# Optimization experiments

Measured on AMD Instinct MI355X. Metric: run time of the kernel, lower is better.

The kernel has to match this reference:

```python
import jax, jax.numpy as jnp
import numpy as np

TEMPERATURE = 10000.0
LN_EPS = 1e-5

def build_freqs(H, W, head_dim):
    # (H*W, head_dim) rotary angles: [theta_h, theta_h, theta_w, theta_w]
    gh, gw = jnp.meshgrid(jnp.arange(H, dtype=jnp.float32), jnp.arange(W, dtype=jnp.float32), indexing='ij')
    dq = head_dim // 4
    freq = 1.0 / (TEMPERATURE ** (jnp.arange(dq, dtype=jnp.float32) / dq))
    th = gh.reshape(-1, 1) * freq[None, :]
    tw = gw.reshape(-1, 1) * freq[None, :]
    return jnp.concatenate([th, th, tw, tw], axis=-1)

def apply_rope(x, freqs):
    # x: (B, nh, N, hd), freqs: (N, hd)
    cos = jnp.cos(freqs)[None, None]
    sin = jnp.sin(freqs)[None, None]
    hd = x.shape[-1]
    x1, x2 = x[..., :hd // 2], x[..., hd // 2:]
    x_rot = jnp.concatenate([-x2, x1], axis=-1)
    return x * cos + x_rot * sin

def setup_inputs() -> dict:
    key = jax.random.key(0)
    ks = jax.random.split(key, 8)
    dim, hidden, B, H, W = 192, 384, 4, 128, 128
    N = H * W
    s = 0.02
    return {
        'x': jax.random.normal(ks[0], (B, N, dim), jnp.float32),
        'in_w': jax.random.normal(ks[1], (hidden, dim), jnp.float32) * s,
        'in_b': jnp.zeros((hidden,), jnp.float32),
        'qkv_w': jax.random.normal(ks[2], (3 * hidden, hidden), jnp.float32) * s,
        'qkv_b': jnp.zeros((3 * hidden,), jnp.float32),
        'lepe_w': jax.random.normal(ks[3], (hidden, 1, 3, 3), jnp.float32) * s,
        'lepe_b': jnp.zeros((hidden,), jnp.float32),
        'ln_g': jnp.ones((hidden,), jnp.float32),
        'ln_b': jnp.zeros((hidden,), jnp.float32),
        'out_w': jax.random.normal(ks[4], (dim, hidden), jnp.float32) * s,
        'out_b': jnp.zeros((dim,), jnp.float32),
        'H': H,
        'W': W,
    }

def reference(x, in_w, in_b, qkv_w, qkv_b, lepe_w, lepe_b, ln_g, ln_b, out_w, out_b, H, W):
    B, N, C = x.shape
    hidden = in_w.shape[0]
    nh = 8
    hd = hidden // nh
    # in_proj: 1x1 conv == per-token linear
    x_seq = jnp.einsum('bnc,hc->bnh', x, in_w) + in_b
    # fused qkv
    qkv = jnp.einsum('bnh,oh->bno', x_seq, qkv_w) + qkv_b
    q, k, v = jnp.split(qkv, 3, axis=-1)
    # LEPE: 3x3 depthwise conv on V in NCHW layout
    v2d = v.transpose(0, 2, 1).reshape(B, hidden, H, W)
    lepe = jax.lax.conv_general_dilated(
        v2d, lepe_w, window_strides=(1, 1), padding=((1, 1), (1, 1)),
        feature_group_count=hidden, dimension_numbers=('NCHW', 'OIHW', 'NCHW'))
    lepe = lepe + lepe_b[None, :, None, None]
    v = v + lepe.reshape(B, hidden, N).transpose(0, 2, 1)
    # split heads -> (B, nh, N, hd)
    q = q.reshape(B, N, nh, hd).transpose(0, 2, 1, 3)
    k = k.reshape(B, N, nh, hd).transpose(0, 2, 1, 3)
    v = v.reshape(B, N, nh, hd).transpose(0, 2, 1, 3)
    freqs = build_freqs(H, W, hd)
    q = apply_rope(q, freqs)
    k = apply_rope(k, freqs)
    # phi = ELU + 1 feature map
    q = jax.nn.elu(q) + 1.0
    k = jax.nn.elu(k) + 1.0
    # linear attention associativity trick
    kv = jnp.einsum('bhnd,bhne->bhde', k, v)
    out = jnp.einsum('bhnd,bhde->bhne', q, kv)
    k_sum = k.sum(axis=2)  # (B, nh, hd)
    denom = jnp.maximum(jnp.einsum('bhnd,bhd->bhn', q, k_sum)[..., None], 1e-6)
    out = out / denom
    out = out.transpose(0, 2, 1, 3).reshape(B, N, hidden)
    # LayerNorm + out_proj
    mu = out.mean(axis=-1, keepdims=True)
    var = out.var(axis=-1, keepdims=True)
    out = (out - mu) * jax.lax.rsqrt(var + LN_EPS) * ln_g + ln_b
    return jnp.einsum('bnh,ch->bnc', out, out_w) + out_b
```

## Files before the change

kernel.cpp:

```cpp
#include <hip/hip_runtime.h>
#include <cstdint>
#include <cstddef>

#define NN_TOK 16384
#define ROWS   65536
#define CDIM   192
#define HID    384
#define NHEAD  8
#define HD     48
#define QKVO   1152

typedef unsigned short ushort_t;
typedef __bf16 bf16x8 __attribute__((ext_vector_type(8)));
typedef float  f32x4  __attribute__((ext_vector_type(4)));

__device__ __forceinline__ ushort_t f2bf(float f) {
  __bf16 h = (__bf16)f;
  ushort_t u;
  __builtin_memcpy(&u, &h, 2);
  return u;
}
__device__ __forceinline__ float bf2f(ushort_t u) {
  return __uint_as_float(((unsigned int)u) << 16);
}

__global__ void cast_x(const float* __restrict__ x, ushort_t* __restrict__ xb, int n8) {
  int i = blockIdx.x * blockDim.x + threadIdx.x;
  if (i >= n8) return;
  const float4* src = (const float4*)(x + (size_t)i * 8);
  float4 f0 = src[0], f1 = src[1];
  uint4 pk;
  pk.x = (unsigned)f2bf(f0.x) | ((unsigned)f2bf(f0.y) << 16);
  pk.y = (unsigned)f2bf(f0.z) | ((unsigned)f2bf(f0.w) << 16);
  pk.z = (unsigned)f2bf(f1.x) | ((unsigned)f2bf(f1.y) << 16);
  pk.w = (unsigned)f2bf(f1.z) | ((unsigned)f2bf(f1.w) << 16);
  *(uint4*)(xb + (size_t)i * 8) = pk;
}

__global__ void combine_w(const float* __restrict__ in_w, const float* __restrict__ in_b,
                          const float* __restrict__ qkv_w, const float* __restrict__ qkv_b,
                          ushort_t* __restrict__ Wcb, float* __restrict__ bc) {
  int o = blockIdx.x;
  int c = threadIdx.x;
  const float* qw = qkv_w + o * HID;
  float s = 0.f;
  for (int m = 0; m < HID; ++m) s += qw[m] * in_w[m * CDIM + c];
  Wcb[o * CDIM + c] = f2bf(s);
  if (c == 0) {
    float sb = qkv_b[o];
    for (int m = 0; m < HID; ++m) sb += qw[m] * in_b[m];
    bc[o] = sb;
  }
}

__global__ void cast_owT(const float* __restrict__ w, ushort_t* __restrict__ wt, int n) {
  int i = blockIdx.x * blockDim.x + threadIdx.x;
  if (i >= n) return;
  int j = i & 7, rest = i >> 3;
  int l15 = rest & 15; rest >>= 4;
  int quad = rest & 3; rest >>= 2;
  int kt = rest % 12, ct = rest / 12;
  int col = ct * 16 + l15, k = kt * 32 + quad * 8 + j;
  wt[i] = f2bf(w[col * HID + k]);
}

__global__ void build_tab(float4* __restrict__ tab4) {
  int i = blockIdx.x * blockDim.x + threadIdx.x;
  if (i >= NN_TOK * 24) return;
  int n = i / 24, dp = i - n * 24;
  int j = dp % 12;
  const float c0 = 1.1073093649624542f;
  float freq = exp2f(-(float)j * c0);
  float fy = (float)(n >> 7), fx = (float)(n & 127);
  float s1, c1, s2, c2;
  sincosf(fy * freq, &s1, &c1);
  sincosf(fx * freq, &s2, &c2);
  tab4[i] = make_float4(c1, s1, c2, s2);
}

template<int BM, int BN, int WM, int WN, bool OUTBF16>
__global__ __launch_bounds__(256) void gemm_mfma(const ushort_t* __restrict__ A, int lda,
                                                 const ushort_t* __restrict__ Wb,
                                                 const float* __restrict__ bias,
                                                 void* __restrict__ Cptr,
                                                 int K, int O, int nbx) {
  constexpr int TM = BM / WM / 16;
  constexpr int TN = BN / WN / 16;
  __shared__ __align__(16) ushort_t As[BM][40];
  __shared__ __align__(16) ushort_t Bs[BN][40];
  const int t    = threadIdx.x;
  const int lane = t & 63;
  const int wave = t >> 6;
  const int quad = lane >> 4;
  const int l15  = lane & 15;
  const int wm   = wave / WN, wn = wave % WN;
  const int m_base = wm * (BM / WM);
  const int n_base = wn * (BN / WN);
  const int cpx = gridDim.x >> 3;
  const int id  = blockIdx.x;
  const int swz = (id & 7) * cpx + (id >> 3);
  const int o0  = (swz % nbx) * BN;
  const int n0  = (swz / nbx) * BM;
  f32x4 acc[TM][TN] = {};

  for (int kt = 0; kt < K; kt += 32) {
    for (int c = t; c < BM * 4; c += 256) {
      int row = c >> 2, col8 = (c & 3) * 8;
      *(uint4*)&As[row][col8] = *(const uint4*)(A + (size_t)(n0 + row) * lda + kt + col8);
    }
    for (int c = t; c < BN * 4; c += 256) {
      int row = c >> 2, col8 = (c & 3) * 8;
      *(uint4*)&Bs[row][col8] = *(const uint4*)(Wb + (size_t)(o0 + row) * K + kt + col8);
    }
    __syncthreads();
    bf16x8 af[TM], bfr[TN];
#pragma unroll
    for (int mi = 0; mi < TM; ++mi)
      af[mi] = *(const bf16x8*)&As[m_base + mi * 16 + l15][quad * 8];
#pragma unroll
    for (int ni = 0; ni < TN; ++ni)
      bfr[ni] = *(const bf16x8*)&Bs[n_base + ni * 16 + l15][quad * 8];
#pragma unroll
    for (int mi = 0; mi < TM; ++mi)
#pragma unroll
      for (int ni = 0; ni < TN; ++ni)
        acc[mi][ni] = __builtin_amdgcn_mfma_f32_16x16x32_bf16(af[mi], bfr[ni], acc[mi][ni], 0, 0, 0);
    __syncthreads();
  }
#pragma unroll
  for (int mi = 0; mi < TM; ++mi) {
#pragma unroll
    for (int ni = 0; ni < TN; ++ni) {
      int col = o0 + n_base + ni * 16 + l15;
      float bv = bias[col];
      int rbase = n0 + m_base + mi * 16 + quad * 4;
#pragma unroll
      for (int r = 0; r < 4; ++r) {
        float val = acc[mi][ni][r] + bv;
        if (OUTBF16) ((ushort_t*)Cptr)[(size_t)(rbase + r) * O + col] = f2bf(val);
        else         ((float*)Cptr)[(size_t)(rbase + r) * O + col] = val;
      }
    }
  }
}

__device__ __forceinline__ int fragEl(int pg, int nb, int dd, int nm) {
  return pg * 2200 + nb * 136 + dd * 8 + nm;
}

__global__ __launch_bounds__(256) void kv_partial_k(const ushort_t* __restrict__ kq,
                                                    const ushort_t* __restrict__ vq,
                                                    const float4* __restrict__ tab4,
                                                    const float* __restrict__ lw,
                                                    const float* __restrict__ lb,
                                                    float* __restrict__ part) {
  const int bid   = blockIdx.x;
  const int chunk = bid & 63;
  const int bh    = bid >> 6;
  const int b     = bh >> 3;
  const int h     = bh & 7;
  const int t     = threadIdx.x;
  const int lane  = t & 63;
  const int wave  = t >> 6;
  __shared__ __align__(16) ushort_t ksR[3 * 2200];
  __shared__ __align__(16) ushort_t vsR[4 * 2200];
  __shared__ __align__(16) float wlds[9][48];
  __shared__ __align__(16) float blds[48];
  float* red = (float*)&ksR[0];
  for (int c = t; c < 432; c += 256) {
    int ch = c / 9, tap = c - ch * 9;
    wlds[tap][ch] = lw[(h * HD + ch) * 9 + tap];
  }
  if (t < 48) blds[t] = lb[h * HD + t];
  for (int c = t; c < 2048; c += 256) {
    int nb = c >> 7, dd = (c >> 3) & 15, nm = c & 7;
    vsR[fragEl(3, nb, dd, nm)] = (dd == 0) ? (ushort_t)0x3F80 : (ushort_t)0;
  }
  __syncthreads();

  const int g  = lane >> 4;
  const int d0 = lane & 15;
  f32x4 acc[3][4] = {};
  const int n0 = b * NN_TOK + chunk * 256;

  for (int it = 0; it < 2; ++it) {
    const int nbase = it * 128;
    for (int c = t; c < 384; c += 256) {
      int rr = c / 3, s8 = (c - (c / 3) * 3) * 8;
      int n  = n0 + nbase + rr;
      int nn = n & (NN_TOK - 1);
      const ushort_t* kr = kq + (size_t)n * QKVO + h * HD;
      uint4 ka = *(const uint4*)(kr + s8);
      uint4 kb = *(const uint4*)(kr + s8 + 24);
      ushort_t ua[8], ub[8];
      *(uint4*)ua = ka; *(uint4*)ub = kb;
      const float4* t4 = tab4 + nn * 24 + s8;
      const int nb = rr >> 3, nm = rr & 7;
#pragma unroll
      for (int jj = 0; jj < 8; ++jj) {
        float4 cs = t4[jj];
        float in1 = bf2f(ua[jj]), in2 = bf2f(ub[jj]);
        float o1 = in1 * cs.x - in2 * cs.y;
        float o2 = in2 * cs.z + in1 * cs.w;
        o1 = (o1 > 0.f) ? o1 + 1.f : __expf(o1);
        o2 = (o2 > 0.f) ? o2 + 1.f : __expf(o2);
        const int d1 = s8 + jj, d2 = s8 + 24 + jj;
        ksR[fragEl(d1 >> 4, nb, d1 & 15, nm)] = f2bf(o1);
        ksR[fragEl(d2 >> 4, nb, d2 & 15, nm)] = f2bf(o2);
      }
    }
    {
      const int nst = chunk * 256 + nbase;
      const int y   = nst >> 7;
      for (int c = t; c < 768; c += 256) {
        int rr = c / 6, gg = c - (c / 6) * 6;
        int x = rr;
        float a8[8], ctr[8];
        *(float4*)&a8[0] = *(const float4*)&blds[gg * 8];
        *(float4*)&a8[4] = *(const float4*)&blds[gg * 8 + 4];
#pragma unroll
        for (int dy = -1; dy <= 1; ++dy) {
#pragma unroll
          for (int dx = -1; dx <= 1; ++dx) {
            int yy = y + dy, xx = x + dx;
            bool inb = ((unsigned)yy < 128u) && ((unsigned)xx < 128u);
            int yc = min(max(yy, 0), 127), xc = min(max(xx, 0), 127);
            const ushort_t* src = vq + ((size_t)(b * NN_TOK + (yc << 7) + xc)) * QKVO + h * HD + gg * 8;
            uint4 pk = *(const uint4*)src;
            if (!inb) pk = make_uint4(0u, 0u, 0u, 0u);
            const int tap = (dy + 1) * 3 + (dx + 1);
            float wt[8];
            *(float4*)&wt[0] = *(const float4*)&wlds[tap][gg * 8];
            *(float4*)&wt[4] = *(const float4*)&wlds[tap][gg * 8 + 4];
            ushort_t uu[8];
            *(uint4*)uu = pk;
#pragma unroll
            for (int ci = 0; ci < 8; ++ci) {
              float val = bf2f(uu[ci]);
              if (dy == 0 && dx == 0) ctr[ci] = val;
              a8[ci] += wt[ci] * val;
            }
          }
        }
        const int nb = rr >> 3, nm = rr & 7;
#pragma unroll
        for (int ci = 0; ci < 8; ++ci) {
          const int e = gg * 8 + ci;
          vsR[fragEl(e >> 4, nb, e & 15, nm)] = f2bf(ctr[ci] + a8[ci]);
        }
      }
    }
    __syncthreads();
    {
      const int w4 = wave * 4 + g;
      bf16x8 af[3], bfr[4];
#pragma unroll
      for (int dg = 0; dg < 3; ++dg) af[dg]  = *(const bf16x8*)&ksR[fragEl(dg, w4, d0, 0)];
#pragma unroll
      for (int eg = 0; eg < 4; ++eg) bfr[eg] = *(const bf16x8*)&vsR[fragEl(eg, w4, d0, 0)];
#pragma unroll
      for (int dg = 0; dg < 3; ++dg)
#pragma unroll
        for (int eg = 0; eg < 4; ++eg)
          acc[dg][eg] = __builtin_amdgcn_mfma_f32_16x16x32_bf16(af[dg], bfr[eg], acc[dg][eg], 0, 0, 0);
    }
    __syncthreads();
  }
  if (wave == 0) {
#pragma unroll
    for (int dg = 0; dg < 3; ++dg)
#pragma unroll
      for (int eg = 0; eg < 4; ++eg)
#pragma unroll
        for (int r = 0; r < 4; ++r)
          red[(dg * 16 + g * 4 + r) * 64 + eg * 16 + d0] = acc[dg][eg][r];
  }
  __syncthreads();
  for (int w = 1; w < 4; ++w) {
    if (wave == w) {
#pragma unroll
      for (int dg = 0; dg < 3; ++dg)
#pragma unroll
        for (int eg = 0; eg < 4; ++eg)
#pragma unroll
          for (int r = 0; r < 4; ++r)
            red[(dg * 16 + g * 4 + r) * 64 + eg * 16 + d0] += acc[dg][eg][r];
    }
    __syncthreads();
  }
  float* p = part + (size_t)bid * 2352;
  for (int c = t; c < 2352; c += 256) {
    int d = c / 49, e = c - d * 49;
    p[c] = red[d * 64 + e];
  }
}

__global__ void kv_phase2(const float* __restrict__ part, ushort_t* __restrict__ kvT) {
  int bh  = blockIdx.x >> 3;
  int seg = blockIdx.x & 7;
  int t   = threadIdx.x;
  ushort_t* dst = kvT + (size_t)bh * 8192;
  for (int i = seg * 1024 + t; i < (seg + 1) * 1024; i += 256) {
    int rem = i & 4095, e = rem >> 6, d = rem & 63;
    if (d >= 48 || e >= 49) dst[i] = 0;
  }
  int cend = (seg + 1) * 294;
  for (int c = seg * 294 + t; c < cend; c += 256) {
    const float* p = part + (size_t)(bh * 64) * 2352 + c;
    float s = 0.f;
    for (int ch = 0; ch < 64; ++ch) s += p[(size_t)ch * 2352];
    int d = c / 49, e = c - d * 49;
    ushort_t hi = f2bf(s);
    float lo = s - bf2f(hi);
    dst[(size_t)e * 64 + d]        = hi;
    dst[4096 + (size_t)e * 64 + d] = f2bf(lo);
  }
}

__global__ __launch_bounds__(256) void attn_ln_fused(const ushort_t* __restrict__ q,
                                                     const float4* __restrict__ tab4,
                                                     const ushort_t* __restrict__ kvT,
                                                     const float* __restrict__ ln_g,
                                                     const float* __restrict__ ln_b,
                                                     const ushort_t* __restrict__ owbT,
                                                     const float* __restrict__ out_b,
                                                     float* __restrict__ outp) {
  __shared__ __align__(16) ushort_t qsL[32][392];
  __shared__ __align__(16) float tabL[32][100];
  __shared__ float lnp[4][32][2];
  const int t    = threadIdx.x;
  const int lane = t & 63;
  const int wave = t >> 6;
  const int quad = lane >> 4;
  const int l15  = lane & 15;
  const int row0 = blockIdx.x * 32;
  const int b    = row0 >> 14;
  const int h0   = wave * 2;

  for (int c = t; c < 1536; c += 256) {
    int r = c / 48, seg = c - (c / 48) * 48;
    *(uint4*)&qsL[r][seg * 8] = *(const uint4*)(q + (size_t)(row0 + r) * QKVO + seg * 8);
  }
  for (int c = t; c < 768; c += 256) {
    int r = c / 24, dp = c - (c / 24) * 24;
    float4 v = tab4[(size_t)(((row0 + r) & (NN_TOK - 1))) * 24 + dp];
    *(float4*)&tabL[r][dp * 4] = v;
  }
  __syncthreads();

  f32x4 acc[2][2][4] = {};

  float gg[2][3], bb[2][3];
#pragma unroll
  for (int hi = 0; hi < 2; ++hi)
#pragma unroll
    for (int nt = 0; nt < 3; ++nt) {
      int col = (h0 + hi) * 48 + nt * 16 + l15;
      gg[hi][nt] = ln_g[col];
      bb[hi][nt] = ln_b[col];
    }

#pragma unroll
  for (int s = 0; s < 2; ++s) {
    const int d0 = s * 32 + quad * 8;
    bf16x8 bfH[2][4], bfL[2][4];
#pragma unroll
    for (int hi = 0; hi < 2; ++hi) {
      const ushort_t* kb = kvT + (size_t)(b * 8 + h0 + hi) * 8192;
#pragma unroll
      for (int nt = 0; nt < 4; ++nt) {
        bfH[hi][nt] = *(const bf16x8*)(kb + (nt * 16 + l15) * 64 + d0);
        bfL[hi][nt] = *(const bf16x8*)(kb + 4096 + (nt * 16 + l15) * 64 + d0);
      }
    }
    const bool valid = d0 < 48;
    const bool caseA = d0 < 24;
    const int dp0 = caseA ? d0 : d0 - 24;
    bf16x8 af[2][2] = {};
    if (valid) {
      const int dpart = caseA ? d0 + 24 : d0 - 24;
      const int csel  = caseA ? 0 : 2;
      const float sgn = caseA ? -1.f : 1.f;
#pragma unroll
      for (int m = 0; m < 2; ++m) {
        const int r = m * 16 + l15;
        float2 cs[8];
#pragma unroll
        for (int j = 0; j < 8; ++j)
          cs[j] = *(const float2*)&tabL[r][(dp0 + j) * 4 + csel];
#pragma unroll
        for (int hi = 0; hi < 2; ++hi) {
          const ushort_t* qr = &qsL[r][(h0 + hi) * 48];
          uint4 pr = *(const uint4*)(qr + d0);
          uint4 pa = *(const uint4*)(qr + dpart);
          ushort_t up[8], ua[8];
          *(uint4*)up = pr; *(uint4*)ua = pa;
          bf16x8 av;
#pragma unroll
          for (int j = 0; j < 8; ++j) {
            float vp = bf2f(up[j]), va = bf2f(ua[j]);
            float o = vp * cs[j].x + va * (sgn * cs[j].y);
            o = (o > 0.f) ? o + 1.f : __expf(o);
            av[j] = (__bf16)o;
          }
          af[hi][m] = av;
        }
      }
    }
#pragma unroll
    for (int hi = 0; hi < 2; ++hi)
#pragma unroll
      for (int nt = 0; nt < 4; ++nt)
#pragma unroll
        for (int m = 0; m < 2; ++m) {
          acc[hi][m][nt] = __builtin_amdgcn_mfma_f32_16x16x32_bf16(af[hi][m], bfH[hi][nt], acc[hi][m][nt], 0, 0, 0);
          acc[hi][m][nt] = __builtin_amdgcn_mfma_f32_16x16x32_bf16(af[hi][m], bfL[hi][nt], acc[hi][m][nt], 0, 0, 0);
        }
  }

  float rdn[2][2][4];
#pragma unroll
  for (int hi = 0; hi < 2; ++hi)
#pragma unroll
    for (int m = 0; m < 2; ++m)
#pragma unroll
      for (int r = 0; r < 4; ++r) {
        float dn = __shfl(acc[hi][m][3][r], lane & 48);
        rdn[hi][m][r] = 1.f / fmaxf(dn, 1e-6f);
      }
  float s1[2][4] = {}, s2[2][4] = {};
#pragma unroll
  for (int hi = 0; hi < 2; ++hi)
#pragma unroll
    for (int m = 0; m < 2; ++m)
#pragma unroll
      for (int nt = 0; nt < 3; ++nt)
#pragma unroll
        for (int r = 0; r < 4; ++r) {
          float o = acc[hi][m][nt][r] * rdn[hi][m][r];
          acc[hi][m][nt][r] = o;
          s1[m][r] += o;
          s2[m][r] += o * o;
        }
#pragma unroll
  for (int m = 0; m < 2; ++m)
#pragma unroll
    for (int r = 0; r < 4; ++r) {
#pragma unroll
      for (int msk = 1; msk < 16; msk <<= 1) {
        s1[m][r] += __shfl_xor(s1[m][r], msk, 64);
        s2[m][r] += __shfl_xor(s2[m][r], msk, 64);
      }
    }
  if (l15 == 0) {
#pragma unroll
    for (int m = 0; m < 2; ++m)
#pragma unroll
      for (int r = 0; r < 4; ++r) {
        int rr = m * 16 + quad * 4 + r;
        lnp[wave][rr][0] = s1[m][r];
        lnp[wave][rr][1] = s2[m][r];
      }
  }
  __syncthreads();
  float muv[2][4], rsv[2][4];
#pragma unroll
  for (int m = 0; m < 2; ++m)
#pragma unroll
    for (int r = 0; r < 4; ++r) {
      int rr = m * 16 + quad * 4 + r;
      float a  = lnp[0][rr][0] + lnp[1][rr][0] + lnp[2][rr][0] + lnp[3][rr][0];
      float bq = lnp[0][rr][1] + lnp[1][rr][1] + lnp[2][rr][1] + lnp[3][rr][1];
      float mu  = a * (1.f / 384.f);
      float var = bq * (1.f / 384.f) - mu * mu;
      muv[m][r] = mu;
      rsv[m][r] = rsqrtf(var + 1e-5f);
    }
#pragma unroll
  for (int hi = 0; hi < 2; ++hi)
#pragma unroll
    for (int m = 0; m < 2; ++m)
#pragma unroll
      for (int nt = 0; nt < 3; ++nt) {
        int col = (h0 + hi) * 48 + nt * 16 + l15;
#pragma unroll
        for (int r = 0; r < 4; ++r) {
          int rr = m * 16 + quad * 4 + r;
          float v = (acc[hi][m][nt][r] - muv[m][r]) * rsv[m][r] * gg[hi][nt] + bb[hi][nt];
          qsL[rr][col] = f2bf(v);
        }
      }
  __syncthreads();

  f32x4 oac[2][3] = {};
  const int ct0 = wave * 3;
  float obv[3];
#pragma unroll
  for (int nt = 0; nt < 3; ++nt) obv[nt] = out_b[ct0 * 16 + nt * 16 + l15];
#pragma unroll
  for (int kt = 0; kt < 12; ++kt) {
    bf16x8 af2[2];
    af2[0] = *(const bf16x8*)&qsL[l15][kt * 32 + quad * 8];
    af2[1] = *(const bf16x8*)&qsL[16 + l15][kt * 32 + quad * 8];
    bf16x8 bfr2[3];
#pragma unroll
    for (int nt = 0; nt < 3; ++nt)
      bfr2[nt] = *(const bf16x8*)&owbT[(size_t)((((ct0 + nt) * 12 + kt) * 4 + quad) * 16 + l15) * 8];
#pragma unroll
    for (int m2 = 0; m2 < 2; ++m2)
#pragma unroll
      for (int nt = 0; nt < 3; ++nt)
        oac[m2][nt] = __builtin_amdgcn_mfma_f32_16x16x32_bf16(af2[m2], bfr2[nt], oac[m2][nt], 0, 0, 0);
  }
  __syncthreads();
  float* coL = (float*)&qsL[0][0];
#pragma unroll
  for (int m2 = 0; m2 < 2; ++m2)
#pragma unroll
    for (int nt = 0; nt < 3; ++nt) {
      int col = ct0 * 16 + nt * 16 + l15;
#pragma unroll
      for (int r = 0; r < 4; ++r)
        coL[(m2 * 16 + quad * 4 + r) * 196 + col] = oac[m2][nt][r] + obv[nt];
    }
  __syncthreads();
  for (int c = t; c < 1536; c += 256) {
    int r = c / 48, seg = c - (c / 48) * 48;
    *(float4*)(outp + (size_t)(row0 + r) * CDIM + seg * 4) = *(const float4*)&coL[r * 196 + seg * 4];
  }
}

extern "C" void kernel_launch(void* const* d_in, const int* in_sizes, int n_in,
                              void* d_out, int out_size, void* d_ws, size_t ws_size,
                              hipStream_t stream) {
  const float* x      = (const float*)d_in[0];
  const float* in_w   = (const float*)d_in[1];
  const float* in_b   = (const float*)d_in[2];
  const float* qkv_w  = (const float*)d_in[3];
  const float* qkv_b  = (const float*)d_in[4];
  const float* lepe_w = (const float*)d_in[5];
  const float* lepe_b = (const float*)d_in[6];
  const float* ln_g   = (const float*)d_in[7];
  const float* ln_b   = (const float*)d_in[8];
  const float* out_w  = (const float*)d_in[9];
  const float* out_b  = (const float*)d_in[10];
  float* out = (float*)d_out;

  float*    ws     = (float*)d_ws;
  float*    qkvbF  = ws;
  float*    xbF    = qkvbF + (size_t)ROWS * QKVO / 2;
  float*    WcbF   = xbF   + (size_t)ROWS * CDIM / 2;
  float*    bc     = WcbF  + (size_t)QKVO * CDIM / 2;
  float*    owbF   = bc    + QKVO;
  float*    tab4F  = owbF  + (size_t)CDIM * HID / 2;
  ushort_t* qkvb   = (ushort_t*)qkvbF;
  ushort_t* xb     = (ushort_t*)xbF;
  float*    part   = xbF;
  ushort_t* kvT    = (ushort_t*)(xbF + (size_t)2048 * 2352);
  ushort_t* Wcb    = (ushort_t*)WcbF;
  ushort_t* owbT   = (ushort_t*)owbF;
  float4*   tab4   = (float4*)tab4F;

  cast_x<<<(ROWS * CDIM / 8 + 255) / 256, 256, 0, stream>>>(x, xb, ROWS * CDIM / 8);
  combine_w<<<QKVO, CDIM, 0, stream>>>(in_w, in_b, qkv_w, qkv_b, Wcb, bc);
  cast_owT<<<(CDIM * HID + 255) / 256, 256, 0, stream>>>(out_w, owbT, CDIM * HID);
  build_tab<<<(NN_TOK * 24 + 255) / 256, 256, 0, stream>>>(tab4);

  gemm_mfma<128, 128, 2, 2, true><<<4608, 256, 0, stream>>>(
      xb, CDIM, Wcb, bc, qkvb, CDIM, QKVO, 9);

  kv_partial_k<<<2048, 256, 0, stream>>>(qkvb + HID, qkvb + 2 * HID, tab4, lepe_w, lepe_b, part);
  kv_phase2<<<256, 256, 0, stream>>>(part, kvT);

  attn_ln_fused<<<ROWS / 32, 256, 0, stream>>>(qkvb, tab4, kvT, ln_g, ln_b, owbT, out_b, out);
}
```

Baseline: 381.3 us.

## Write K and V head-major from QKV GEMM epilogue for contiguous per-head reads

The QKV GEMM epilogue now splits its output into a token-major Q buffer of width 384 and head-major K and V buffers laid out (B*heads, N, 48). The kv_partial kernel then reads each head's K/V rows contiguously (96-byte rows) instead of striding through 1152-wide rows, which should improve cache-line use and reduce fetched bytes. The attention kernel reads Q from the narrower buffer. The trade-off is that epilogue stores for K/V are scattered by head, and the workspace layout grows and shifts.

After: 382.8 us. Within noise of the previous version (+0.4%).

```diff
diff --git a/kernel.cpp b/kernel.cpp
--- a/kernel.cpp
+++ b/kernel.cpp
@@ -78,12 +78,14 @@
   tab4[i] = make_float4(c1, s1, c2, s2);
 }
 
-template<int BM, int BN, int WM, int WN, bool OUTBF16>
-__global__ __launch_bounds__(256) void gemm_mfma(const ushort_t* __restrict__ A, int lda,
-                                                 const ushort_t* __restrict__ Wb,
-                                                 const float* __restrict__ bias,
-                                                 void* __restrict__ Cptr,
-                                                 int K, int O, int nbx) {
+template<int BM, int BN, int WM, int WN>
+__global__ __launch_bounds__(256) void gemm_qkv(const ushort_t* __restrict__ A, int lda,
+                                                const ushort_t* __restrict__ Wb,
+                                                const float* __restrict__ bias,
+                                                ushort_t* __restrict__ qb,
+                                                ushort_t* __restrict__ kTb,
+                                                ushort_t* __restrict__ vTb,
+                                                int K, int nbx) {
   constexpr int TM = BM / WM / 16;
   constexpr int TN = BN / WN / 16;
   __shared__ __align__(16) ushort_t As[BM][40];
@@ -134,11 +136,21 @@
       int col = o0 + n_base + ni * 16 + l15;
       float bv = bias[col];
       int rbase = n0 + m_base + mi * 16 + quad * 4;
-#pragma unroll
-      for (int r = 0; r < 4; ++r) {
-        float val = acc[mi][ni][r] + bv;
-        if (OUTBF16) ((ushort_t*)Cptr)[(size_t)(rbase + r) * O + col] = f2bf(val);
-        else         ((float*)Cptr)[(size_t)(rbase + r) * O + col] = val;
+      if (col < HID) {
+#pragma unroll
+        for (int r = 0; r < 4; ++r)
+          qb[(size_t)(rbase + r) * HID + col] = f2bf(acc[mi][ni][r] + bv);
+      } else {
+        int co = col - HID;
+        ushort_t* dp = kTb;
+        if (co >= HID) { co -= HID; dp = vTb; }
+        int hh = co / 48, dd = co - hh * 48;
+#pragma unroll
+        for (int r = 0; r < 4; ++r) {
+          int row = rbase + r;
+          int bb = row >> 14, n = row & (NN_TOK - 1);
+          dp[((size_t)(bb * 8 + hh) * NN_TOK + n) * 48 + dd] = f2bf(acc[mi][ni][r] + bv);
+        }
       }
     }
   }
@@ -157,7 +169,6 @@
   const int bid   = blockIdx.x;
   const int chunk = bid & 63;
   const int bh    = bid >> 6;
-  const int b     = bh >> 3;
   const int h     = bh & 7;
   const int t     = threadIdx.x;
   const int lane  = t & 63;
@@ -181,20 +192,20 @@
   const int g  = lane >> 4;
   const int d0 = lane & 15;
   f32x4 acc[3][4] = {};
-  const int n0 = b * NN_TOK + chunk * 256;
+  const size_t hbase = (size_t)bh * NN_TOK * 48;
+  const int nst0 = chunk * 256;
 
   for (int it = 0; it < 2; ++it) {
     const int nbase = it * 128;
     for (int c = t; c < 384; c += 256) {
       int rr = c / 3, s8 = (c - (c / 3) * 3) * 8;
-      int n  = n0 + nbase + rr;
-      int nn = n & (NN_TOK - 1);
-      const ushort_t* kr = kq + (size_t)n * QKVO + h * HD;
+      int nl = nst0 + nbase + rr;
+      const ushort_t* kr = kq + hbase + (size_t)nl * 48;
       uint4 ka = *(const uint4*)(kr + s8);
       uint4 kb = *(const uint4*)(kr + s8 + 24);
       ushort_t ua[8], ub[8];
       *(uint4*)ua = ka; *(uint4*)ub = kb;
-      const float4* t4 = tab4 + nn * 24 + s8;
+      const float4* t4 = tab4 + nl * 24 + s8;
       const int nb = rr >> 3, nm = rr & 7;
 #pragma unroll
       for (int jj = 0; jj < 8; ++jj) {
@@ -210,8 +221,7 @@
       }
     }
     {
-      const int nst = chunk * 256 + nbase;
-      const int y   = nst >> 7;
+      const int y = (nst0 + nbase) >> 7;
       for (int c = t; c < 768; c += 256) {
         int rr = c / 6, gg = c - (c / 6) * 6;
         int x = rr;
@@ -225,7 +235,7 @@
             int yy = y + dy, xx = x + dx;
             bool inb = ((unsigned)yy < 128u) && ((unsigned)xx < 128u);
             int yc = min(max(yy, 0), 127), xc = min(max(xx, 0), 127);
-            const ushort_t* src = vq + ((size_t)(b * NN_TOK + (yc << 7) + xc)) * QKVO + h * HD + gg * 8;
+            const ushort_t* src = vq + hbase + (size_t)((yc << 7) + xc) * 48 + gg * 8;
             uint4 pk = *(const uint4*)src;
             if (!inb) pk = make_uint4(0u, 0u, 0u, 0u);
             const int tap = (dy + 1) * 3 + (dx + 1);
@@ -317,7 +327,7 @@
   }
 }
 
-__global__ __launch_bounds__(256) void attn_ln_fused(const ushort_t* __restrict__ q,
+__global__ __launch_bounds__(256) void attn_ln_fused(const ushort_t* __restrict__ qb,
                                                      const float4* __restrict__ tab4,
                                                      const ushort_t* __restrict__ kvT,
                                                      const float* __restrict__ ln_g,
@@ -339,7 +349,7 @@
 
   for (int c = t; c < 1536; c += 256) {
     int r = c / 48, seg = c - (c / 48) * 48;
-    *(uint4*)&qsL[r][seg * 8] = *(const uint4*)(q + (size_t)(row0 + r) * QKVO + seg * 8);
+    *(uint4*)&qsL[r][seg * 8] = *(const uint4*)(qb + (size_t)(row0 + r) * HID + seg * 8);
   }
   for (int c = t; c < 768; c += 256) {
     int r = c / 24, dp = c - (c / 24) * 24;
@@ -547,13 +557,17 @@
   float* out = (float*)d_out;
 
   float*    ws     = (float*)d_ws;
-  float*    qkvbF  = ws;
-  float*    xbF    = qkvbF + (size_t)ROWS * QKVO / 2;
-  float*    WcbF   = xbF   + (size_t)ROWS * CDIM / 2;
-  float*    bc     = WcbF  + (size_t)QKVO * CDIM / 2;
-  float*    owbF   = bc    + QKVO;
-  float*    tab4F  = owbF  + (size_t)CDIM * HID / 2;
-  ushort_t* qkvb   = (ushort_t*)qkvbF;
+  float*    qbF    = ws;
+  float*    kTF    = qbF  + (size_t)ROWS * HID / 2;
+  float*    vTF    = kTF  + (size_t)ROWS * HID / 2;
+  float*    xbF    = vTF  + (size_t)ROWS * HID / 2;
+  float*    WcbF   = xbF  + (size_t)ROWS * CDIM / 2;
+  float*    bc     = WcbF + (size_t)QKVO * CDIM / 2;
+  float*    owbF   = bc   + QKVO;
+  float*    tab4F  = owbF + (size_t)CDIM * HID / 2;
+  ushort_t* qb     = (ushort_t*)qbF;
+  ushort_t* kTb    = (ushort_t*)kTF;
+  ushort_t* vTb    = (ushort_t*)vTF;
   ushort_t* xb     = (ushort_t*)xbF;
   float*    part   = xbF;
   ushort_t* kvT    = (ushort_t*)(xbF + (size_t)2048 * 2352);
@@ -566,11 +580,11 @@
   cast_owT<<<(CDIM * HID + 255) / 256, 256, 0, stream>>>(out_w, owbT, CDIM * HID);
   build_tab<<<(NN_TOK * 24 + 255) / 256, 256, 0, stream>>>(tab4);
 
-  gemm_mfma<128, 128, 2, 2, true><<<4608, 256, 0, stream>>>(
-      xb, CDIM, Wcb, bc, qkvb, CDIM, QKVO, 9);
-
-  kv_partial_k<<<2048, 256, 0, stream>>>(qkvb + HID, qkvb + 2 * HID, tab4, lepe_w, lepe_b, part);
+  gemm_qkv<128, 128, 2, 2><<<4608, 256, 0, stream>>>(
+      xb, CDIM, Wcb, bc, qb, kTb, vTb, CDIM, 9);
+
+  kv_partial_k<<<2048, 256, 0, stream>>>(kTb, vTb, tab4, lepe_w, lepe_b, part);
   kv_phase2<<<256, 256, 0, stream>>>(part, kvT);
 
-  attn_ln_fused<<<ROWS / 32, 256, 0, stream>>>(qkvb, tab4, kvT, ln_g, ln_b, owbT, out_b, out);
-}
+  attn_ln_fused<<<ROWS / 32, 256, 0, stream>>>(qb, tab4, kvT, ln_g, ln_b, owbT, out_b, out);
+}
```
